# Kernel tuning notes

Hardware: AMD Instinct MI355X
Metric: run time of the kernel (lower is better)

The kernel has to match this reference:

```python
import math
import jax, jax.numpy as jnp
import numpy as np

D_MODEL = 256
NUM_HEAD = 8
NUM_LEVEL = 1
KERNEL = 5
NUM_POINT = KERNEL * KERNEL
NUM_VAR = 5  # with_rotation=True
HEAD_DIM = D_MODEL // NUM_HEAD


def _kernel_indices(k=KERNEL):
    # odd kernel: linspace(-(k-1)/2, (k-1)/2, k); torch.meshgrid default 'ij'; stack([j,i])/k
    idx = jnp.linspace(-(k - 1) / 2.0, (k - 1) / 2.0, k)
    ii, jj = jnp.meshgrid(idx, idx, indexing='ij')
    return jnp.stack([jj, ii], axis=-1).reshape(-1, 2) / k  # (P, 2)


def setup_inputs() -> dict:
    key = jax.random.key(0)
    ks = jax.random.split(key, 8)
    B, LQ = 2, 4096
    Hf, Wf = 188, 188
    LV = Hf * Wf
    d = D_MODEL
    nb = NUM_LEVEL * NUM_HEAD * NUM_VAR
    na = NUM_HEAD * NUM_LEVEL * NUM_POINT
    return {
        'query': jax.random.normal(ks[0], (B, LQ, d), jnp.float32),
        'value': jax.random.normal(ks[1], (B, LV, d), jnp.float32),
        'ref_windows': jax.random.uniform(ks[2], (B, LQ, 7), jnp.float32),
        'W_box': jax.random.normal(ks[3], (nb, d), jnp.float32) * 0.02,
        'b_box': jax.random.uniform(ks[4], (nb,), jnp.float32),
        'W_attn': jax.random.normal(ks[5], (na, d), jnp.float32) * 0.02,
        'b_attn': jnp.zeros((na,), jnp.float32),
        'W_value': jax.random.normal(ks[6], (d, d), jnp.float32) * 0.02,
        'b_value': jnp.zeros((d,), jnp.float32),
        'W_out': jax.random.normal(ks[7], (d, d), jnp.float32) * 0.02,
        'b_out': jnp.zeros((d,), jnp.float32),
        'H_feat': Hf,
        'W_feat': Wf,
    }


def reference(query, value, ref_windows, W_box, b_box, W_attn, b_attn,
              W_value, b_value, W_out, b_out, H_feat, W_feat):
    B, LQ, d = query.shape
    LV = value.shape[1]
    Hh, Lv, P, Dh = NUM_HEAD, NUM_LEVEL, NUM_POINT, HEAD_DIM

    # value projection -> (B, LV, Hh, Dh)
    v = (value @ W_value.T + b_value).reshape(B, LV, Hh, Dh)

    # attention weights: softmax over (level*point) per head
    attn = jax.nn.softmax((query @ W_attn.T + b_attn).reshape(B, LQ, Hh, Lv * P), axis=-1)
    attn = attn.reshape(B, LQ, Hh, Lv, P)

    # --- _where_to_attend ---
    ob = (query @ W_box.T + b_box).reshape(B, LQ, Hh, Lv, NUM_VAR)
    rw = ref_windows[:, :, None, None, :]                    # (B,LQ,1,1,7)
    ref_boxes = rw[..., jnp.array([0, 1, 3, 4])]             # cx, cy, w, h
    ref_angles = rw[..., 6:7]
    off_boxes, off_angles = ob[..., :4], ob[..., 4:5]
    angles = (ref_angles + off_angles / 16.0) * (2.0 * math.pi)
    boxes = ref_boxes + off_boxes / 8.0 * ref_boxes[..., jnp.array([2, 3, 2, 3])]
    center = boxes[..., None, :2]                            # (B,LQ,Hh,Lv,1,2)
    size = boxes[..., None, 2:4]
    cos_a, sin_a = jnp.cos(angles), jnp.sin(angles)
    rot = jnp.stack([cos_a, -sin_a, sin_a, cos_a], axis=-1).reshape(B, LQ, Hh, Lv, 1, 2, 2)
    g = _kernel_indices() * jax.nn.relu(size)                # (B,LQ,Hh,Lv,P,2)
    grid = center + (g[..., None, :] * rot).sum(-1)          # (B,LQ,Hh,Lv,P,2), normalized [0,1]

    # --- single-level bilinear sampling (align_corners=False, zero padding) ---
    gl = grid[:, :, :, 0]                                    # (B,LQ,Hh,P,2)
    gx = gl[..., 0] * W_feat - 0.5
    gy = gl[..., 1] * H_feat - 0.5
    x0 = jnp.floor(gx)
    y0 = jnp.floor(gy)
    x0i = x0.astype(jnp.int32)
    y0i = y0.astype(jnp.int32)
    wx1 = gx - x0
    wy1 = gy - y0
    wx0 = 1.0 - wx1
    wy0 = 1.0 - wy1

    b_idx = jnp.arange(B)[:, None, None, None]
    h_idx = jnp.arange(Hh)[None, None, :, None]

    def gather(yi, xi):
        valid = (xi >= 0) & (xi < W_feat) & (yi >= 0) & (yi < H_feat)
        lin = jnp.clip(yi, 0, H_feat - 1) * W_feat + jnp.clip(xi, 0, W_feat - 1)
        return v[b_idx, lin, h_idx] * valid[..., None]       # (B,LQ,Hh,P,Dh)

    s = (gather(y0i, x0i) * (wy0 * wx0)[..., None]
         + gather(y0i, x0i + 1) * (wy0 * wx1)[..., None]
         + gather(y0i + 1, x0i) * (wy1 * wx0)[..., None]
         + gather(y0i + 1, x0i + 1) * (wy1 * wx1)[..., None])

    out_heads = (s * attn[:, :, :, 0, :, None]).sum(axis=3)  # (B,LQ,Hh,Dh)
    out = out_heads.reshape(B, LQ, Hh * Dh) @ W_out.T + b_out
    attn_w = attn.reshape(B, LQ, Hh, Lv, KERNEL, KERNEL)
    return out, attn_w
```

## Files before the change

kernel.cpp:

```cpp
#include <hip/hip_runtime.h>


typedef float floatx4 __attribute__((ext_vector_type(4)));
typedef short shortx8 __attribute__((ext_vector_type(8)));

static __device__ __forceinline__ unsigned short f2bf(float x) {
    unsigned int u = __float_as_uint(x);
    return (unsigned short)((u + 0x7fffu + ((u >> 16) & 1u)) >> 16);
}
static __device__ __forceinline__ unsigned int pack2(float a, float b) {
    return (unsigned int)f2bf(a) | ((unsigned int)f2bf(b) << 16);
}
static __device__ __forceinline__ void async16(const void* g, void* lds) {
    __builtin_amdgcn_global_load_lds(
        (const __attribute__((address_space(1))) unsigned int*)g,
        (__attribute__((address_space(3))) unsigned int*)lds, 16, 0, 0);
}

__global__ __launch_bounds__(256) void convert_kernel(
    const float* __restrict__ W_value, unsigned short* __restrict__ wvbf,
    const float* __restrict__ W_attn, const float* __restrict__ W_box,
    float* __restrict__ Wab,
    const float* __restrict__ W_out, unsigned short* __restrict__ wobf,
    const float* __restrict__ b_attn, const float* __restrict__ b_box,
    float* __restrict__ bab)
{
    const int blk = blockIdx.x, tid = threadIdx.x;
    if (blk < 16) {
        int base = blk * 1024 + tid;
#pragma unroll
        for (int k = 0; k < 4; ++k) {
            int j = base + k * 256;
            float4 f = ((const float4*)W_value)[j];
            ((uint2*)wvbf)[j] = make_uint2(pack2(f.x, f.y), pack2(f.z, f.w));
        }
    } else if (blk < 32) {
        int base = (blk - 16) * 1024 + tid;
#pragma unroll
        for (int k = 0; k < 4; ++k) {
            int j = base + k * 256;
            int row = j >> 6, col = (j & 63) * 4;
            float4 f;
            if (row < 200)      f = *(const float4*)(W_attn + (size_t)row * 256 + col);
            else if (row < 240) f = *(const float4*)(W_box + (size_t)(row - 200) * 256 + col);
            else                f = make_float4(0.f, 0.f, 0.f, 0.f);
            ((float4*)Wab)[j] = f;
        }
    } else if (blk < 48) {
        int base = (blk - 32) * 1024 + tid;
#pragma unroll
        for (int k = 0; k < 4; ++k) {
            int j = base + k * 256;
            float4 f = ((const float4*)W_out)[j];
            ((uint2*)wobf)[j] = make_uint2(pack2(f.x, f.y), pack2(f.z, f.w));
        }
    } else {
        bab[tid] = tid < 200 ? b_attn[tid] : (tid < 240 ? b_box[tid - 200] : 0.f);
    }
}

template <int OUTMODE, int AFP32, int BM>
__global__ __launch_bounds__(256) void gemm_bf16(
    const void* __restrict__ Av,
    const unsigned short* __restrict__ Bw,
    const float* __restrict__ bias,
    void* __restrict__ Cv, int M, int LV)
{
    constexpr int NI = BM / 32;
    constexpr int TI = BM / 32;
    __shared__ unsigned short As[2][BM * 64];
    __shared__ unsigned short Bs[2][128 * 64];
    const int tid = threadIdx.x;
    const int wv = tid >> 6, lane = tid & 63;
    const int lr = lane & 15, lq = lane >> 4;
    const int m0 = blockIdx.x * BM, n0 = blockIdx.y * 128;
    const int wm = wv & 1, wn = wv >> 1;
    const int srow = tid >> 3;
    const int colg = tid & 7;
    const int colgSw = colg ^ (srow & 7);
    const int dstA = (srow * 8 + colgSw) * 16;

    floatx4 acc[TI][4];
#pragma unroll
    for (int i = 0; i < TI; ++i)
#pragma unroll
        for (int j = 0; j < 4; ++j) acc[i][j] = (floatx4){0.f, 0.f, 0.f, 0.f};

    float4 ar0[NI], ar1[NI];

    if constexpr (AFP32) {
        const float* Af = (const float*)Av;
#pragma unroll
        for (int i = 0; i < NI; ++i) {
            int ra = m0 + i * 32 + srow; ra = ra < M ? ra : M - 1;
            const float* ap = Af + (size_t)ra * 256 + colg * 8;
            ar0[i] = *(const float4*)ap;
            ar1[i] = *(const float4*)(ap + 4);
        }
    } else {
        const unsigned short* Ab = (const unsigned short*)Av;
#pragma unroll
        for (int i = 0; i < NI; ++i) {
            int ra = m0 + i * 32 + srow; ra = ra < M ? ra : M - 1;
            async16(Ab + (size_t)ra * 256 + colgSw * 8, (char*)As[0] + i * 4096 + wv * 1024);
        }
    }
#pragma unroll
    for (int i = 0; i < 4; ++i) {
        int rb = n0 + i * 32 + srow;
        async16(Bw + (size_t)rb * 256 + colgSw * 8, (char*)Bs[0] + i * 4096 + wv * 1024);
    }
    if constexpr (AFP32) {
#pragma unroll
        for (int i = 0; i < NI; ++i) {
            uint4 pv = make_uint4(pack2(ar0[i].x, ar0[i].y), pack2(ar0[i].z, ar0[i].w),
                                  pack2(ar1[i].x, ar1[i].y), pack2(ar1[i].z, ar1[i].w));
            *(uint4*)((char*)As[0] + i * 4096 + dstA) = pv;
        }
    }
    __syncthreads();

    int cur = 0;
    for (int kc = 0; kc < 4; ++kc) {
        const int nk = (kc + 1) * 64;
        if (kc < 3) {
            if constexpr (AFP32) {
                const float* Af = (const float*)Av;
#pragma unroll
                for (int i = 0; i < NI; ++i) {
                    int ra = m0 + i * 32 + srow; ra = ra < M ? ra : M - 1;
                    const float* ap = Af + (size_t)ra * 256 + nk + colg * 8;
                    ar0[i] = *(const float4*)ap;
                    ar1[i] = *(const float4*)(ap + 4);
                }
            } else {
                const unsigned short* Ab = (const unsigned short*)Av;
#pragma unroll
                for (int i = 0; i < NI; ++i) {
                    int ra = m0 + i * 32 + srow; ra = ra < M ? ra : M - 1;
                    async16(Ab + (size_t)ra * 256 + nk + colgSw * 8,
                            (char*)As[cur ^ 1] + i * 4096 + wv * 1024);
                }
            }
#pragma unroll
            for (int i = 0; i < 4; ++i) {
                int rb = n0 + i * 32 + srow;
                async16(Bw + (size_t)rb * 256 + nk + colgSw * 8,
                        (char*)Bs[cur ^ 1] + i * 4096 + wv * 1024);
            }
        }
#pragma unroll
        for (int kb = 0; kb < 2; ++kb) {
            shortx8 af[TI], bfr[4];
#pragma unroll
            for (int t = 0; t < TI; ++t) {
                int arow = wm * (BM / 2) + t * 16 + lr;
                af[t] = *(const shortx8*)&As[cur][arow * 64 + (((kb * 4 + lq) ^ (arow & 7)) * 8)];
            }
#pragma unroll
            for (int t = 0; t < 4; ++t) {
                int brow = wn * 64 + t * 16 + lr;
                bfr[t] = *(const shortx8*)&Bs[cur][brow * 64 + (((kb * 4 + lq) ^ (brow & 7)) * 8)];
            }
#pragma unroll
            for (int ti = 0; ti < TI; ++ti)
#pragma unroll
                for (int tj = 0; tj < 4; ++tj)
                    acc[ti][tj] = __builtin_amdgcn_mfma_f32_16x16x32_bf16(bfr[tj], af[ti], acc[ti][tj], 0, 0, 0);
        }
        if (kc < 3) {
            if constexpr (AFP32) {
#pragma unroll
                for (int i = 0; i < NI; ++i) {
                    uint4 pv = make_uint4(pack2(ar0[i].x, ar0[i].y), pack2(ar0[i].z, ar0[i].w),
                                          pack2(ar1[i].x, ar1[i].y), pack2(ar1[i].z, ar1[i].w));
                    *(uint4*)((char*)As[cur ^ 1] + i * 4096 + dstA) = pv;
                }
            }
        }
        __syncthreads();
        cur ^= 1;
    }
#pragma unroll
    for (int ti = 0; ti < TI; ++ti) {
        int m = m0 + wm * (BM / 2) + ti * 16 + lr;
        if (m >= M) continue;
        if (OUTMODE == 0) {
            float* Crow = (float*)Cv + (size_t)m * 256;
#pragma unroll
            for (int tj = 0; tj < 4; ++tj) {
                int nb = n0 + wn * 64 + tj * 16 + lq * 4;
                float4 bv = *(const float4*)(bias + nb);
                float4 o = make_float4(acc[ti][tj][0] + bv.x, acc[ti][tj][1] + bv.y,
                                       acc[ti][tj][2] + bv.z, acc[ti][tj][3] + bv.w);
                *(float4*)(Crow + nb) = o;
            }
        } else {
            int b = m >= LV ? 1 : 0;
            int lv = m - (b ? LV : 0);
#pragma unroll
            for (int tj = 0; tj < 4; ++tj) {
                int nb = n0 + wn * 64 + tj * 16 + lq * 4;
                float4 bv = *(const float4*)(bias + nb);
                int h = nb >> 5, dh = nb & 31;
                unsigned short* dst = (unsigned short*)Cv + ((size_t)(b * 8 + h) * LV + lv) * 32 + dh;
                *(uint2*)dst = make_uint2(pack2(acc[ti][tj][0] + bv.x, acc[ti][tj][1] + bv.y),
                                          pack2(acc[ti][tj][2] + bv.z, acc[ti][tj][3] + bv.w));
            }
        }
    }
}

__global__ __launch_bounds__(256) void gemm_nt_bias(
    const float* __restrict__ A, const float* __restrict__ W,
    const float* __restrict__ bias, float* __restrict__ C, int M)
{
    const int K = 256, N = 256;
    __shared__ float As[16][68];
    __shared__ float Bs[16][68];
    int tid = threadIdx.x;
    int tcol = tid & 15, trow = tid >> 4;
    int m0 = blockIdx.x * 64, n0 = blockIdx.y * 64;
    int lr = tid >> 2, lc = (tid & 3) << 2;
    float acc[4][4] = {};
    for (int k0 = 0; k0 < K; k0 += 16) {
        int arow = m0 + lr; if (arow > M - 1) arow = M - 1;
        float4 av = *(const float4*)(A + (size_t)arow * K + k0 + lc);
        float4 wv = *(const float4*)(W + (size_t)(n0 + lr) * K + k0 + lc);
        __syncthreads();
        As[lc + 0][lr] = av.x; As[lc + 1][lr] = av.y; As[lc + 2][lr] = av.z; As[lc + 3][lr] = av.w;
        Bs[lc + 0][lr] = wv.x; Bs[lc + 1][lr] = wv.y; Bs[lc + 2][lr] = wv.z; Bs[lc + 3][lr] = wv.w;
        __syncthreads();
#pragma unroll
        for (int k = 0; k < 16; ++k) {
            float4 a4 = *(const float4*)&As[k][trow << 2];
            float4 b4 = *(const float4*)&Bs[k][tcol << 2];
            float a[4] = {a4.x, a4.y, a4.z, a4.w};
            float bb[4] = {b4.x, b4.y, b4.z, b4.w};
#pragma unroll
            for (int i = 0; i < 4; i++)
#pragma unroll
                for (int j = 0; j < 4; j++) acc[i][j] += a[i] * bb[j];
        }
    }
#pragma unroll
    for (int i = 0; i < 4; i++) {
        int m = m0 + trow * 4 + i;
        if (m >= M) continue;
#pragma unroll
        for (int j = 0; j < 4; j++) {
            int n = n0 + tcol * 4 + j;
            C[(size_t)m * N + n] = acc[i][j] + bias[n];
        }
    }
}

__global__ __launch_bounds__(256) void decode_sample_kernel(
    const unsigned short* __restrict__ v,
    const float* __restrict__ logits,
    const float* __restrict__ ref_windows,
    float* __restrict__ attn_out,
    unsigned short* __restrict__ ohbf,
    const int* __restrict__ Hf_p, const int* __restrict__ Wf_p, int LV, int LQ)
{
    __shared__ float lg[8][32];
    __shared__ float rw[8][7];
    __shared__ float prm[8][6];
    __shared__ float mxinv[8][2];
    __shared__ uint4 pk[8][25][2];

    const int lin = blockIdx.y * 16 + blockIdx.x;
    const int nc = gridDim.y;
    const int seq = lin >> 3;
    const int c = seq % nc;
    const int s = (lin & 7) + ((seq / nc) << 3);
    const int b = s >> 3, h = s & 7;
    const int tid = threadIdx.x;
    const int Hf = *Hf_p, Wf = *Wf_p;
    const size_t mbase = (size_t)b * LQ + c * 8;

    if (tid < 240) {
        int qq = tid / 30, j = tid - qq * 30;
        int col = (j < 25) ? h * 25 + j : 200 + h * 5 + (j - 25);
        lg[qq][j] = logits[(mbase + qq) * 256 + col];
    }
    if (tid < 56) {
        int qq = tid / 7, k = tid - qq * 7;
        rw[qq][k] = ref_windows[(mbase + qq) * 7 + k];
    }
    __syncthreads();

    if (tid < 8) {
        int qq = tid;
        float mx = -1e30f;
#pragma unroll
        for (int p = 0; p < 25; p++) mx = fmaxf(mx, lg[qq][p]);
        float ssum = 0.f;
#pragma unroll
        for (int p = 0; p < 25; p++) ssum += expf(lg[qq][p] - mx);
        mxinv[qq][0] = mx; mxinv[qq][1] = 1.f / ssum;
        float cx = rw[qq][0] + lg[qq][25] * 0.125f * rw[qq][3];
        float cy = rw[qq][1] + lg[qq][26] * 0.125f * rw[qq][4];
        float bw = rw[qq][3] + lg[qq][27] * 0.125f * rw[qq][3];
        float bh = rw[qq][4] + lg[qq][28] * 0.125f * rw[qq][4];
        float ang = (rw[qq][6] + lg[qq][29] * 0.0625f) * 6.283185307179586f;
        prm[qq][0] = cx; prm[qq][1] = cy;
        prm[qq][2] = fmaxf(bw, 0.f); prm[qq][3] = fmaxf(bh, 0.f);
        prm[qq][4] = cosf(ang); prm[qq][5] = sinf(ang);
    }
    __syncthreads();

    if (tid < 200) {
        int qq = tid / 25, p = tid - qq * 25;
        float a = expf(lg[qq][p] - mxinv[qq][0]) * mxinv[qq][1];
        attn_out[(mbase + qq) * 200 + h * 25 + p] = a;
        int pi = p / 5, pj = p - pi * 5;
        float g0 = (float)(pj - 2) * 0.2f * prm[qq][2];
        float g1 = (float)(pi - 2) * 0.2f * prm[qq][3];
        float ca = prm[qq][4], sa = prm[qq][5];
        float gx = (prm[qq][0] + g0 * ca - g1 * sa) * (float)Wf - 0.5f;
        float gy = (prm[qq][1] + g0 * sa + g1 * ca) * (float)Hf - 0.5f;
        float x0f = floorf(gx), y0f = floorf(gy);
        int x0 = (int)x0f, y0 = (int)y0f;
        float wx1 = gx - x0f, wy1 = gy - y0f;
        float wx0 = 1.f - wx1, wy0 = 1.f - wy1;
        int y1 = y0 + 1;
        int bx; float wl, wr;
        if (x0 >= 0 && x0 <= Wf - 2)      { bx = x0;     wl = wx0; wr = wx1; }
        else if (x0 == -1)                { bx = 0;      wl = wx1; wr = 0.f; }
        else if (x0 == Wf - 1)            { bx = Wf - 2; wl = 0.f; wr = wx0; }
        else                              { bx = 0;      wl = 0.f; wr = 0.f; }
        float wy0v = (y0 >= 0 && y0 < Hf) ? wy0 : 0.f;
        float wy1v = (y1 >= 0 && y1 < Hf) ? wy1 : 0.f;
        int cy0 = min(max(y0, 0), Hf - 1), cy1 = min(max(y1, 0), Hf - 1);
        unsigned off0 = (unsigned)(cy0 * Wf + bx) * 16u;
        unsigned off1 = (unsigned)(cy1 * Wf + bx) * 16u;
        float aw0 = a * wy0v, aw1 = a * wy1v;
        pk[qq][p][0] = make_uint4(__float_as_uint(aw0 * wl), __float_as_uint(aw1 * wl), off0, off1);
        pk[qq][p][1] = make_uint4(__float_as_uint(aw0 * wr), __float_as_uint(aw1 * wr), off0, off1);
    }
    __syncthreads();

    const int qq = tid >> 5, l = tid & 31;
    const unsigned int* vw = (const unsigned int*)(v + (size_t)s * LV * 32);
    const uint4* pkp = &pk[qq][0][l >> 4];
    float e0 = 0.f, o0 = 0.f, e1 = 0.f, o1 = 0.f;
#pragma unroll
    for (int p = 0; p < 25; ++p) {
        uint4 t = pkp[2 * p];
        float w0 = __uint_as_float(t.x), w1 = __uint_as_float(t.y);
        unsigned u0 = vw[t.z + l];
        unsigned u1 = vw[t.w + l];
        e0 += w0 * __uint_as_float(u0 << 16);
        o0 += w0 * __uint_as_float(u0 & 0xffff0000u);
        e1 += w1 * __uint_as_float(u1 << 16);
        o1 += w1 * __uint_as_float(u1 & 0xffff0000u);
    }
    float a0 = e0 + e1, a1 = o0 + o1;
    a0 += __shfl_xor(a0, 16, 32);
    a1 += __shfl_xor(a1, 16, 32);
    if (l < 16)
        ((unsigned int*)ohbf)[(mbase + qq) * 128 + h * 16 + l] = pack2(a0, a1);
}

extern "C" void kernel_launch(void* const* d_in, const int* in_sizes, int n_in,
                              void* d_out, int out_size, void* d_ws, size_t ws_size,
                              hipStream_t stream) {
    const float* query       = (const float*)d_in[0];
    const float* value       = (const float*)d_in[1];
    const float* ref_windows = (const float*)d_in[2];
    const float* W_box       = (const float*)d_in[3];
    const float* b_box       = (const float*)d_in[4];
    const float* W_attn      = (const float*)d_in[5];
    const float* b_attn      = (const float*)d_in[6];
    const float* W_value     = (const float*)d_in[7];
    const float* b_value     = (const float*)d_in[8];
    const float* W_out       = (const float*)d_in[9];
    const float* b_out       = (const float*)d_in[10];
    const int*   Hf          = (const int*)d_in[11];
    const int*   Wf          = (const int*)d_in[12];

    const int M1 = in_sizes[1] / 256;
    const int MQ = in_sizes[0] / 256;
    const int LQ = MQ / 2;
    const int LV = M1 / 2;

    unsigned short* Vout = (unsigned short*)d_ws;
    unsigned short* ohbf = Vout + (size_t)M1 * 256;
    unsigned short* wvbf = ohbf + (size_t)MQ * 256;
    unsigned short* wobf = wvbf + 65536;
    float* Wab       = (float*)(wobf + 65536);
    float* bab       = Wab + 65536;
    float* logits    = bab + 256;

    float* out0     = (float*)d_out;
    float* attn_out = out0 + (size_t)MQ * 256;

    convert_kernel<<<49, 256, 0, stream>>>(W_value, wvbf, W_attn, W_box, Wab,
                                           W_out, wobf, b_attn, b_box, bab);
    dim3 g1((M1 + 127) / 128, 2);
    gemm_bf16<1, 1, 128><<<g1, 256, 0, stream>>>(value, wvbf, b_value, Vout, M1, LV);
    dim3 g2(MQ / 64, 4);
    gemm_nt_bias<<<g2, 256, 0, stream>>>(query, Wab, bab, logits, MQ);
    decode_sample_kernel<<<dim3(16, LQ / 8), 256, 0, stream>>>(
        Vout, logits, ref_windows, attn_out, ohbf, Hf, Wf, LV, LQ);
    dim3 g4(MQ / 64, 2);
    gemm_bf16<0, 0, 64><<<g4, 256, 0, stream>>>(ohbf, wobf, b_out, out0, MQ, LV);
}
```

Before: 217.9 us.

## Deepen fp32 A-operand prefetch in GEMM with manual waitcnt and sched barriers

For the fp32-A GEMM path, the k-loop is restructured so global loads of the next-next A chunk are issued in registers two stages ahead, and B async loads one stage ahead. Explicit s_waitcnt vmcnt/lgkmcnt and raw s_barrier calls with sched_barrier fences replace __syncthreads, so outstanding A prefetches need not drain at each barrier. The intent is to hide global load latency behind MFMA compute in the value-projection GEMM. The risk is fragile hand-counted vmcnt values and extra register pressure.

```diff
diff --git a/kernel.cpp b/kernel.cpp
--- a/kernel.cpp
+++ b/kernel.cpp
@@ -3,6 +3,11 @@
 
 typedef float floatx4 __attribute__((ext_vector_type(4)));
 typedef short shortx8 __attribute__((ext_vector_type(8)));
+
+#define SB0 __builtin_amdgcn_sched_barrier(0)
+#define VMCNT8 asm volatile("s_waitcnt vmcnt(8)" ::: "memory")
+#define VMCNT0 asm volatile("s_waitcnt vmcnt(0)" ::: "memory")
+#define LGKM0  asm volatile("s_waitcnt lgkmcnt(0)" ::: "memory")
 
 static __device__ __forceinline__ unsigned short f2bf(float x) {
     unsigned int u = __float_as_uint(x);
@@ -86,101 +91,131 @@
 #pragma unroll
         for (int j = 0; j < 4; ++j) acc[i][j] = (floatx4){0.f, 0.f, 0.f, 0.f};
 
-    float4 ar0[NI], ar1[NI];
+    auto compute = [&](const unsigned short* Acur, const unsigned short* Bcur) {
+#pragma unroll
+        for (int kb = 0; kb < 2; ++kb) {
+            shortx8 af[TI], bfr[4];
+#pragma unroll
+            for (int t = 0; t < TI; ++t) {
+                int arow = wm * (BM / 2) + t * 16 + lr;
+                af[t] = *(const shortx8*)&Acur[arow * 64 + (((kb * 4 + lq) ^ (arow & 7)) * 8)];
+            }
+#pragma unroll
+            for (int t = 0; t < 4; ++t) {
+                int brow = wn * 64 + t * 16 + lr;
+                bfr[t] = *(const shortx8*)&Bcur[brow * 64 + (((kb * 4 + lq) ^ (brow & 7)) * 8)];
+            }
+#pragma unroll
+            for (int ti = 0; ti < TI; ++ti)
+#pragma unroll
+                for (int tj = 0; tj < 4; ++tj)
+                    acc[ti][tj] = __builtin_amdgcn_mfma_f32_16x16x32_bf16(bfr[tj], af[ti], acc[ti][tj], 0, 0, 0);
+        }
+    };
 
     if constexpr (AFP32) {
         const float* Af = (const float*)Av;
+        const float* aptr[NI];
 #pragma unroll
         for (int i = 0; i < NI; ++i) {
             int ra = m0 + i * 32 + srow; ra = ra < M ? ra : M - 1;
-            const float* ap = Af + (size_t)ra * 256 + colg * 8;
-            ar0[i] = *(const float4*)ap;
-            ar1[i] = *(const float4*)(ap + 4);
-        }
-    } else {
-        const unsigned short* Ab = (const unsigned short*)Av;
-#pragma unroll
-        for (int i = 0; i < NI; ++i) {
-            int ra = m0 + i * 32 + srow; ra = ra < M ? ra : M - 1;
-            async16(Ab + (size_t)ra * 256 + colgSw * 8, (char*)As[0] + i * 4096 + wv * 1024);
-        }
-    }
-#pragma unroll
-    for (int i = 0; i < 4; ++i) {
-        int rb = n0 + i * 32 + srow;
-        async16(Bw + (size_t)rb * 256 + colgSw * 8, (char*)Bs[0] + i * 4096 + wv * 1024);
-    }
-    if constexpr (AFP32) {
+            aptr[i] = Af + (size_t)ra * 256 + colg * 8;
+        }
+        const unsigned short* bptr = Bw + (size_t)(n0 + srow) * 256 + colgSw * 8;
+        float4 ar0[NI], ar1[NI];
+
+#pragma unroll
+        for (int i = 0; i < NI; ++i) { ar0[i] = *(const float4*)aptr[i]; ar1[i] = *(const float4*)(aptr[i] + 4); }
+#pragma unroll
+        for (int i = 0; i < 4; ++i)
+            async16(bptr + (size_t)i * 8192, (char*)Bs[0] + i * 4096 + wv * 1024);
+        SB0;
 #pragma unroll
         for (int i = 0; i < NI; ++i) {
             uint4 pv = make_uint4(pack2(ar0[i].x, ar0[i].y), pack2(ar0[i].z, ar0[i].w),
                                   pack2(ar1[i].x, ar1[i].y), pack2(ar1[i].z, ar1[i].w));
             *(uint4*)((char*)As[0] + i * 4096 + dstA) = pv;
         }
-    }
-    __syncthreads();
-
-    int cur = 0;
-    for (int kc = 0; kc < 4; ++kc) {
-        const int nk = (kc + 1) * 64;
-        if (kc < 3) {
-            if constexpr (AFP32) {
-                const float* Af = (const float*)Av;
+#pragma unroll
+        for (int i = 0; i < NI; ++i) { ar0[i] = *(const float4*)(aptr[i] + 64); ar1[i] = *(const float4*)(aptr[i] + 68); }
+        SB0;
+        VMCNT8;
+        LGKM0;
+        __builtin_amdgcn_s_barrier();
+        SB0;
+
+#pragma unroll
+        for (int kc = 0; kc < 4; ++kc) {
+            const int cur = kc & 1;
+            if (kc < 3) {
+#pragma unroll
+                for (int i = 0; i < 4; ++i)
+                    async16(bptr + (size_t)i * 8192 + (kc + 1) * 64,
+                            (char*)Bs[cur ^ 1] + i * 4096 + wv * 1024);
+            }
+            SB0;
+            compute(As[cur], Bs[cur]);
+            SB0;
+            if (kc < 3) {
 #pragma unroll
                 for (int i = 0; i < NI; ++i) {
-                    int ra = m0 + i * 32 + srow; ra = ra < M ? ra : M - 1;
-                    const float* ap = Af + (size_t)ra * 256 + nk + colg * 8;
-                    ar0[i] = *(const float4*)ap;
-                    ar1[i] = *(const float4*)(ap + 4);
+                    uint4 pv = make_uint4(pack2(ar0[i].x, ar0[i].y), pack2(ar0[i].z, ar0[i].w),
+                                          pack2(ar1[i].x, ar1[i].y), pack2(ar1[i].z, ar1[i].w));
+                    *(uint4*)((char*)As[cur ^ 1] + i * 4096 + dstA) = pv;
                 }
-            } else {
-                const unsigned short* Ab = (const unsigned short*)Av;
+                if (kc < 2) {
+#pragma unroll
+                    for (int i = 0; i < NI; ++i) {
+                        ar0[i] = *(const float4*)(aptr[i] + (kc + 2) * 64);
+                        ar1[i] = *(const float4*)(aptr[i] + (kc + 2) * 64 + 4);
+                    }
+                    SB0;
+                    VMCNT8;
+                } else {
+                    SB0;
+                    VMCNT0;
+                }
+                LGKM0;
+                __builtin_amdgcn_s_barrier();
+                SB0;
+            }
+        }
+    } else {
+        const unsigned short* Ab = (const unsigned short*)Av;
+#pragma unroll
+        for (int i = 0; i < NI; ++i) {
+            int ra = m0 + i * 32 + srow; ra = ra < M ? ra : M - 1;
+            async16(Ab + (size_t)ra * 256 + colgSw * 8, (char*)As[0] + i * 4096 + wv * 1024);
+        }
+#pragma unroll
+        for (int i = 0; i < 4; ++i) {
+            int rb = n0 + i * 32 + srow;
+            async16(Bw + (size_t)rb * 256 + colgSw * 8, (char*)Bs[0] + i * 4096 + wv * 1024);
+        }
+        __syncthreads();
+        int cur = 0;
+        for (int kc = 0; kc < 4; ++kc) {
+            const int nk = (kc + 1) * 64;
+            if (kc < 3) {
 #pragma unroll
                 for (int i = 0; i < NI; ++i) {
                     int ra = m0 + i * 32 + srow; ra = ra < M ? ra : M - 1;
                     async16(Ab + (size_t)ra * 256 + nk + colgSw * 8,
                             (char*)As[cur ^ 1] + i * 4096 + wv * 1024);
                 }
-            }
-#pragma unroll
-            for (int i = 0; i < 4; ++i) {
-                int rb = n0 + i * 32 + srow;
-                async16(Bw + (size_t)rb * 256 + nk + colgSw * 8,
-                        (char*)Bs[cur ^ 1] + i * 4096 + wv * 1024);
-            }
-        }
-#pragma unroll
-        for (int kb = 0; kb < 2; ++kb) {
-            shortx8 af[TI], bfr[4];
-#pragma unroll
-            for (int t = 0; t < TI; ++t) {
-                int arow = wm * (BM / 2) + t * 16 + lr;
-                af[t] = *(const shortx8*)&As[cur][arow * 64 + (((kb * 4 + lq) ^ (arow & 7)) * 8)];
-            }
-#pragma unroll
-            for (int t = 0; t < 4; ++t) {
-                int brow = wn * 64 + t * 16 + lr;
-                bfr[t] = *(const shortx8*)&Bs[cur][brow * 64 + (((kb * 4 + lq) ^ (brow & 7)) * 8)];
-            }
-#pragma unroll
-            for (int ti = 0; ti < TI; ++ti)
-#pragma unroll
-                for (int tj = 0; tj < 4; ++tj)
-                    acc[ti][tj] = __builtin_amdgcn_mfma_f32_16x16x32_bf16(bfr[tj], af[ti], acc[ti][tj], 0, 0, 0);
-        }
-        if (kc < 3) {
-            if constexpr (AFP32) {
-#pragma unroll
-                for (int i = 0; i < NI; ++i) {
-                    uint4 pv = make_uint4(pack2(ar0[i].x, ar0[i].y), pack2(ar0[i].z, ar0[i].w),
-                                          pack2(ar1[i].x, ar1[i].y), pack2(ar1[i].z, ar1[i].w));
-                    *(uint4*)((char*)As[cur ^ 1] + i * 4096 + dstA) = pv;
+#pragma unroll
+                for (int i = 0; i < 4; ++i) {
+                    int rb = n0 + i * 32 + srow;
+                    async16(Bw + (size_t)rb * 256 + nk + colgSw * 8,
+                            (char*)Bs[cur ^ 1] + i * 4096 + wv * 1024);
                 }
             }
-        }
-        __syncthreads();
-        cur ^= 1;
-    }
+            compute(As[cur], Bs[cur]);
+            __syncthreads();
+            cur ^= 1;
+        }
+    }
+
 #pragma unroll
     for (int ti = 0; ti < TI; ++ti) {
         int m = m0 + wm * (BM / 2) + ti * 16 + lr;
```

Result: faster. 212.4 us (-2.5%).

## Use persistent value-projection GEMM with full weight resident in LDS

Applied to the files above, without the earlier changes.

The value projection GEMM becomes a persistent kernel of 256 blocks with 512 threads. Each block loads the entire 256x256 bf16 W_value into padded LDS once, then loops over 64-row tiles of the fp32 value matrix. A fragments are read straight from global memory and converted to bf16 in registers, with no LDS staging or double buffering. This removes the repeated B-tile loads and per-k-chunk syncs and makes each A row be read only once instead of once per N-half, at the cost of about 135KB of LDS per block (one block per CU) and global-load latency that is not hidden by async prefetch. The output GEMM is split into its own non-templated kernel with unchanged behaviour.

```diff
diff --git a/kernel.cpp b/kernel.cpp
--- a/kernel.cpp
+++ b/kernel.cpp
@@ -59,15 +59,97 @@
     }
 }
 
-template <int OUTMODE, int AFP32, int BM>
-__global__ __launch_bounds__(256) void gemm_bf16(
-    const void* __restrict__ Av,
+__global__ __launch_bounds__(512) void gemm_vproj(
+    const float* __restrict__ A,
     const unsigned short* __restrict__ Bw,
     const float* __restrict__ bias,
-    void* __restrict__ Cv, int M, int LV)
+    unsigned short* __restrict__ Vout, int M, int LV)
 {
-    constexpr int NI = BM / 32;
-    constexpr int TI = BM / 32;
+    __shared__ unsigned short Bs[256 * 264];
+    const int tid = threadIdx.x;
+    const int wv = tid >> 6, lane = tid & 63;
+    const int lr = lane & 15, lq = lane >> 4;
+    const int wn = wv & 3, wm = wv >> 2;
+
+#pragma unroll
+    for (int it = 0; it < 16; ++it) {
+        int j = it * 512 + tid;
+        int row = j >> 5, gc = j & 31;
+        uint4 v = *(const uint4*)(Bw + (size_t)row * 256 + gc * 8);
+        *(uint4*)((char*)Bs + row * 528 + gc * 16) = v;
+    }
+    __syncthreads();
+
+    int bbase[4];
+#pragma unroll
+    for (int t = 0; t < 4; ++t) {
+        int rb = wn * 64 + t * 16 + lr;
+        bbase[t] = rb * 528 + lq * 16;
+    }
+
+    const int niter = (M + 63) / 64;
+    for (int it = blockIdx.x; it < niter; it += gridDim.x) {
+        const float* ap[2];
+#pragma unroll
+        for (int t = 0; t < 2; ++t) {
+            int ra = it * 64 + wm * 32 + t * 16 + lr;
+            ra = ra < M ? ra : M - 1;
+            ap[t] = A + (size_t)ra * 256 + lq * 8;
+        }
+        floatx4 acc[2][4];
+#pragma unroll
+        for (int i = 0; i < 2; ++i)
+#pragma unroll
+            for (int j = 0; j < 4; ++j) acc[i][j] = (floatx4){0.f, 0.f, 0.f, 0.f};
+
+#pragma unroll
+        for (int ks = 0; ks < 8; ++ks) {
+            shortx8 af[2], bf[4];
+#pragma unroll
+            for (int t = 0; t < 4; ++t)
+                bf[t] = *(const shortx8*)((const char*)Bs + bbase[t] + ks * 64);
+#pragma unroll
+            for (int t = 0; t < 2; ++t) {
+                float4 f0 = *(const float4*)(ap[t] + ks * 32);
+                float4 f1 = *(const float4*)(ap[t] + ks * 32 + 4);
+                union { uint4 u; shortx8 s; } cv;
+                cv.u = make_uint4(pack2(f0.x, f0.y), pack2(f0.z, f0.w),
+                                  pack2(f1.x, f1.y), pack2(f1.z, f1.w));
+                af[t] = cv.s;
+            }
+#pragma unroll
+            for (int ti = 0; ti < 2; ++ti)
+#pragma unroll
+                for (int tj = 0; tj < 4; ++tj)
+                    acc[ti][tj] = __builtin_amdgcn_mfma_f32_16x16x32_bf16(bf[tj], af[ti], acc[ti][tj], 0, 0, 0);
+        }
+#pragma unroll
+        for (int ti = 0; ti < 2; ++ti) {
+            int m = it * 64 + wm * 32 + ti * 16 + lr;
+            if (m >= M) continue;
+            int b = m >= LV ? 1 : 0;
+            int lv = m - (b ? LV : 0);
+#pragma unroll
+            for (int tj = 0; tj < 4; ++tj) {
+                int nb = wn * 64 + tj * 16 + lq * 4;
+                float4 bv = *(const float4*)(bias + nb);
+                int h = nb >> 5, dh = nb & 31;
+                unsigned short* dst = Vout + ((size_t)(b * 8 + h) * LV + lv) * 32 + dh;
+                *(uint2*)dst = make_uint2(pack2(acc[ti][tj][0] + bv.x, acc[ti][tj][1] + bv.y),
+                                          pack2(acc[ti][tj][2] + bv.z, acc[ti][tj][3] + bv.w));
+            }
+        }
+    }
+}
+
+__global__ __launch_bounds__(256) void gemm_out(
+    const unsigned short* __restrict__ Ab,
+    const unsigned short* __restrict__ Bw,
+    const float* __restrict__ bias,
+    float* __restrict__ C, int M)
+{
+    constexpr int BM = 64;
+    constexpr int NI = BM / 32, TI = BM / 32;
     __shared__ unsigned short As[2][BM * 64];
     __shared__ unsigned short Bs[2][128 * 64];
     const int tid = threadIdx.x;
@@ -78,7 +160,6 @@
     const int srow = tid >> 3;
     const int colg = tid & 7;
     const int colgSw = colg ^ (srow & 7);
-    const int dstA = (srow * 8 + colgSw) * 16;
 
     floatx4 acc[TI][4];
 #pragma unroll
@@ -86,61 +167,48 @@
 #pragma unroll
         for (int j = 0; j < 4; ++j) acc[i][j] = (floatx4){0.f, 0.f, 0.f, 0.f};
 
-    float4 ar0[NI], ar1[NI];
-
-    if constexpr (AFP32) {
-        const float* Af = (const float*)Av;
-#pragma unroll
-        for (int i = 0; i < NI; ++i) {
-            int ra = m0 + i * 32 + srow; ra = ra < M ? ra : M - 1;
-            const float* ap = Af + (size_t)ra * 256 + colg * 8;
-            ar0[i] = *(const float4*)ap;
-            ar1[i] = *(const float4*)(ap + 4);
-        }
-    } else {
-        const unsigned short* Ab = (const unsigned short*)Av;
-#pragma unroll
-        for (int i = 0; i < NI; ++i) {
-            int ra = m0 + i * 32 + srow; ra = ra < M ? ra : M - 1;
-            async16(Ab + (size_t)ra * 256 + colgSw * 8, (char*)As[0] + i * 4096 + wv * 1024);
-        }
+    auto compute = [&](const unsigned short* Acur, const unsigned short* Bcur) {
+#pragma unroll
+        for (int kb = 0; kb < 2; ++kb) {
+            shortx8 af[TI], bfr[4];
+#pragma unroll
+            for (int t = 0; t < TI; ++t) {
+                int arow = wm * (BM / 2) + t * 16 + lr;
+                af[t] = *(const shortx8*)&Acur[arow * 64 + (((kb * 4 + lq) ^ (arow & 7)) * 8)];
+            }
+#pragma unroll
+            for (int t = 0; t < 4; ++t) {
+                int brow = wn * 64 + t * 16 + lr;
+                bfr[t] = *(const shortx8*)&Bcur[brow * 64 + (((kb * 4 + lq) ^ (brow & 7)) * 8)];
+            }
+#pragma unroll
+            for (int ti = 0; ti < TI; ++ti)
+#pragma unroll
+                for (int tj = 0; tj < 4; ++tj)
+                    acc[ti][tj] = __builtin_amdgcn_mfma_f32_16x16x32_bf16(bfr[tj], af[ti], acc[ti][tj], 0, 0, 0);
+        }
+    };
+
+#pragma unroll
+    for (int i = 0; i < NI; ++i) {
+        int ra = m0 + i * 32 + srow; ra = ra < M ? ra : M - 1;
+        async16(Ab + (size_t)ra * 256 + colgSw * 8, (char*)As[0] + i * 4096 + wv * 1024);
     }
 #pragma unroll
     for (int i = 0; i < 4; ++i) {
         int rb = n0 + i * 32 + srow;
         async16(Bw + (size_t)rb * 256 + colgSw * 8, (char*)Bs[0] + i * 4096 + wv * 1024);
     }
-    if constexpr (AFP32) {
-#pragma unroll
-        for (int i = 0; i < NI; ++i) {
-            uint4 pv = make_uint4(pack2(ar0[i].x, ar0[i].y), pack2(ar0[i].z, ar0[i].w),
-                                  pack2(ar1[i].x, ar1[i].y), pack2(ar1[i].z, ar1[i].w));
-            *(uint4*)((char*)As[0] + i * 4096 + dstA) = pv;
-        }
-    }
     __syncthreads();
-
     int cur = 0;
     for (int kc = 0; kc < 4; ++kc) {
         const int nk = (kc + 1) * 64;
         if (kc < 3) {
-            if constexpr (AFP32) {
-                const float* Af = (const float*)Av;
-#pragma unroll
-                for (int i = 0; i < NI; ++i) {
-                    int ra = m0 + i * 32 + srow; ra = ra < M ? ra : M - 1;
-                    const float* ap = Af + (size_t)ra * 256 + nk + colg * 8;
-                    ar0[i] = *(const float4*)ap;
-                    ar1[i] = *(const float4*)(ap + 4);
-                }
-            } else {
-                const unsigned short* Ab = (const unsigned short*)Av;
-#pragma unroll
-                for (int i = 0; i < NI; ++i) {
-                    int ra = m0 + i * 32 + srow; ra = ra < M ? ra : M - 1;
-                    async16(Ab + (size_t)ra * 256 + nk + colgSw * 8,
-                            (char*)As[cur ^ 1] + i * 4096 + wv * 1024);
-                }
+#pragma unroll
+            for (int i = 0; i < NI; ++i) {
+                int ra = m0 + i * 32 + srow; ra = ra < M ? ra : M - 1;
+                async16(Ab + (size_t)ra * 256 + nk + colgSw * 8,
+                        (char*)As[cur ^ 1] + i * 4096 + wv * 1024);
             }
 #pragma unroll
             for (int i = 0; i < 4; ++i) {
@@ -149,35 +217,7 @@
                         (char*)Bs[cur ^ 1] + i * 4096 + wv * 1024);
             }
         }
-#pragma unroll
-        for (int kb = 0; kb < 2; ++kb) {
-            shortx8 af[TI], bfr[4];
-#pragma unroll
-            for (int t = 0; t < TI; ++t) {
-                int arow = wm * (BM / 2) + t * 16 + lr;
-                af[t] = *(const shortx8*)&As[cur][arow * 64 + (((kb * 4 + lq) ^ (arow & 7)) * 8)];
-            }
-#pragma unroll
-            for (int t = 0; t < 4; ++t) {
-                int brow = wn * 64 + t * 16 + lr;
-                bfr[t] = *(const shortx8*)&Bs[cur][brow * 64 + (((kb * 4 + lq) ^ (brow & 7)) * 8)];
-            }
-#pragma unroll
-            for (int ti = 0; ti < TI; ++ti)
-#pragma unroll
-                for (int tj = 0; tj < 4; ++tj)
-                    acc[ti][tj] = __builtin_amdgcn_mfma_f32_16x16x32_bf16(bfr[tj], af[ti], acc[ti][tj], 0, 0, 0);
-        }
-        if (kc < 3) {
-            if constexpr (AFP32) {
-#pragma unroll
-                for (int i = 0; i < NI; ++i) {
-                    uint4 pv = make_uint4(pack2(ar0[i].x, ar0[i].y), pack2(ar0[i].z, ar0[i].w),
-                                          pack2(ar1[i].x, ar1[i].y), pack2(ar1[i].z, ar1[i].w));
-                    *(uint4*)((char*)As[cur ^ 1] + i * 4096 + dstA) = pv;
-                }
-            }
-        }
+        compute(As[cur], Bs[cur]);
         __syncthreads();
         cur ^= 1;
     }
@@ -185,28 +225,14 @@
     for (int ti = 0; ti < TI; ++ti) {
         int m = m0 + wm * (BM / 2) + ti * 16 + lr;
         if (m >= M) continue;
-        if (OUTMODE == 0) {
-            float* Crow = (float*)Cv + (size_t)m * 256;
-#pragma unroll
-            for (int tj = 0; tj < 4; ++tj) {
-                int nb = n0 + wn * 64 + tj * 16 + lq * 4;
-                float4 bv = *(const float4*)(bias + nb);
-                float4 o = make_float4(acc[ti][tj][0] + bv.x, acc[ti][tj][1] + bv.y,
-                                       acc[ti][tj][2] + bv.z, acc[ti][tj][3] + bv.w);
-                *(float4*)(Crow + nb) = o;
-            }
-        } else {
-            int b = m >= LV ? 1 : 0;
-            int lv = m - (b ? LV : 0);
-#pragma unroll
-            for (int tj = 0; tj < 4; ++tj) {
-                int nb = n0 + wn * 64 + tj * 16 + lq * 4;
-                float4 bv = *(const float4*)(bias + nb);
-                int h = nb >> 5, dh = nb & 31;
-                unsigned short* dst = (unsigned short*)Cv + ((size_t)(b * 8 + h) * LV + lv) * 32 + dh;
-                *(uint2*)dst = make_uint2(pack2(acc[ti][tj][0] + bv.x, acc[ti][tj][1] + bv.y),
-                                          pack2(acc[ti][tj][2] + bv.z, acc[ti][tj][3] + bv.w));
-            }
+        float* Crow = C + (size_t)m * 256;
+#pragma unroll
+        for (int tj = 0; tj < 4; ++tj) {
+            int nb = n0 + wn * 64 + tj * 16 + lq * 4;
+            float4 bv = *(const float4*)(bias + nb);
+            float4 o = make_float4(acc[ti][tj][0] + bv.x, acc[ti][tj][1] + bv.y,
+                                   acc[ti][tj][2] + bv.z, acc[ti][tj][3] + bv.w);
+            *(float4*)(Crow + nb) = o;
         }
     }
 }
@@ -398,12 +424,11 @@
 
     convert_kernel<<<49, 256, 0, stream>>>(W_value, wvbf, W_attn, W_box, Wab,
                                            W_out, wobf, b_attn, b_box, bab);
-    dim3 g1((M1 + 127) / 128, 2);
-    gemm_bf16<1, 1, 128><<<g1, 256, 0, stream>>>(value, wvbf, b_value, Vout, M1, LV);
+    gemm_vproj<<<256, 512, 0, stream>>>(value, wvbf, b_value, Vout, M1, LV);
     dim3 g2(MQ / 64, 4);
     gemm_nt_bias<<<g2, 256, 0, stream>>>(query, Wab, bab, logits, MQ);
     decode_sample_kernel<<<dim3(16, LQ / 8), 256, 0, stream>>>(
         Vout, logits, ref_windows, attn_out, ohbf, Hf, Wf, LV, LQ);
     dim3 g4(MQ / 64, 2);
-    gemm_bf16<0, 0, 64><<<g4, 256, 0, stream>>>(ohbf, wobf, b_out, out0, MQ, LV);
-}
+    gemm_out<<<g4, 256, 0, stream>>>(ohbf, wobf, b_out, out0, MQ);
+}
```

Measured after the change: 229.2 us. 5.2% more time.
